# Kernel optimization log

Measured on AMD Instinct MI355X. Metric: run time of the kernel, lower is better.

Reference implementation:

```python
import jax, jax.numpy as jnp
import numpy as np

# Model constants (match init_kwargs)
B, V, NUM_NODES, NUM_RELS = 32, 20, 4000, 400
EMB, HID, L, N, E, OUT = 128, 128, 3, 32000, 256000, 128
DECAY = 0.03
EPS = 0.0  # self_attn eps, not trained


def setup_inputs() -> dict:
    key = jax.random.key(0)
    ks = jax.random.split(key, 20)
    s = 0.02
    return {
        "node_ids": jax.random.randint(ks[0], (N,), 0, NUM_NODES),
        "rel_ids": jax.random.randint(ks[1], (E,), 0, NUM_RELS),
        "edge_index": jax.random.randint(ks[2], (2, E), 0, N),
        "batch": jnp.sort(jax.random.randint(ks[3], (N,), 0, B)),
        "visit_node": jax.random.uniform(ks[4], (B, V, NUM_NODES), dtype=jnp.float32),
        "ehr_nodes": jax.random.uniform(ks[5], (B, NUM_NODES), dtype=jnp.float32),
        "node_emb": jax.random.normal(ks[6], (NUM_NODES, EMB), dtype=jnp.float32) * s,
        "rel_emb": jax.random.normal(ks[7], (NUM_RELS, EMB), dtype=jnp.float32) * s,
        "lin_w": jax.random.normal(ks[8], (HID, EMB), dtype=jnp.float32) * s,
        "lin_b": jnp.zeros((HID,), jnp.float32),
        "alpha_w": jax.random.normal(ks[9], (L, NUM_NODES, NUM_NODES), dtype=jnp.float32) * 0.002,
        "alpha_b": jnp.zeros((L, NUM_NODES), jnp.float32),
        "beta_w": jax.random.normal(ks[10], (L, 1, NUM_NODES), dtype=jnp.float32) * s,
        "beta_b": jnp.zeros((L, 1), jnp.float32),
        "wr_w": jax.random.normal(ks[11], (L, 1, HID), dtype=jnp.float32) * s,
        "wr_b": jnp.zeros((L, 1), jnp.float32),
        "nn_w": jax.random.normal(ks[12], (L, HID, HID), dtype=jnp.float32) * s,
        "nn_b": jnp.zeros((L, HID), jnp.float32),
        "mlp_w": jax.random.normal(ks[13], (OUT, 2 * HID), dtype=jnp.float32) * s,
        "mlp_b": jnp.zeros((OUT,), jnp.float32),
    }


def reference(node_ids, rel_ids, edge_index, batch, visit_node, ehr_nodes,
              node_emb, rel_emb, lin_w, lin_b, alpha_w, alpha_b, beta_w, beta_b,
              wr_w, wr_b, nn_w, nn_b, mlp_w, mlp_b):
    # visit decay weights lambda_j: (1, V, 1)
    lambda_j = jnp.exp(DECAY * (V - jnp.arange(V, dtype=jnp.float32))).reshape(1, V, 1)

    x = node_emb[node_ids] @ lin_w.T + lin_b          # (N, HID)
    edge_attr = rel_emb[rel_ids] @ lin_w.T + lin_b    # (E, HID)
    src, dst = edge_index[0], edge_index[1]
    nid_src = node_ids[src]
    b_src = batch[src]

    for l in range(L):
        # alpha: softmax over visit dim, (B, V, NUM_NODES)
        alpha = jax.nn.softmax(
            jnp.einsum('bvn,mn->bvm', visit_node, alpha_w[l]) + alpha_b[l], axis=1)
        # beta: (B, V, 1) with visit decay
        beta = jnp.tanh(
            jnp.einsum('bvn,on->bvo', visit_node, beta_w[l]) + beta_b[l]) * lambda_j
        attn = jnp.sum(alpha * beta, axis=1)          # (B, NUM_NODES)
        e_attn = attn[b_src, nid_src][:, None]        # (E, 1) per-edge attention

        # BiAttentionGNNConv message: relu(x_j * attn + W_R(edge_attr) * edge_attr)
        w_rel = edge_attr @ wr_w[l].T + wr_b[l]       # (E, 1)
        msg = jax.nn.relu(x[src] * e_attn + w_rel * edge_attr)
        agg = jax.ops.segment_sum(msg, dst, num_segments=N)  # scatter-add aggregate
        out = agg + (1.0 + EPS) * x                   # eps residual
        x = jax.nn.relu(out @ nn_w[l].T + nn_b[l])    # conv.nn Linear + outer relu

    # graph-level patient embedding: global mean pool over batch
    counts = jnp.maximum(
        jax.ops.segment_sum(jnp.ones((N, 1), x.dtype), batch, num_segments=B), 1.0)
    x_graph = jax.ops.segment_sum(x, batch, num_segments=B) / counts  # (B, HID)

    # node-level patient embedding: ehr multihot average of node embeddings
    x_node = (ehr_nodes @ node_emb) / jnp.sum(ehr_nodes, axis=1, keepdims=True)
    x_node = x_node @ lin_w.T + lin_b                 # (B, HID)

    logits = jnp.concatenate([x_graph, x_node], axis=1) @ mlp_w.T + mlp_b
    return logits
```

## Files before the change

### kernel.cpp

```cpp
#include <hip/hip_runtime.h>

namespace {

constexpr int kNodes = 4000;
constexpr int kRels  = 400;
constexpr int kB     = 32;
constexpr int kV     = 20;
constexpr int kN     = 32000;
constexpr int kE     = 256000;
constexpr int kH     = 128;
constexpr int kL     = 3;
constexpr int kMPad  = 4096;
constexpr int kKW    = 4000;
constexpr int kBV    = kB * kV;
constexpr int kNB    = 32;
constexpr int kChunk = kE / kNB;
constexpr int kHalf  = 16000;
constexpr int kPSeg  = 16;
constexpr int kESeg  = 32;

typedef __attribute__((ext_vector_type(8))) short bf16x8;
typedef __attribute__((ext_vector_type(4))) float f32x4;

__device__ inline unsigned short f2bf(float f){
  unsigned int u = __float_as_uint(f);
  u += 0x7FFFu + ((u >> 16) & 1u);
  return (unsigned short)(u >> 16);
}
__device__ inline float bf2f(unsigned short u){
  return __uint_as_float(((unsigned int)u) << 16);
}

__device__ inline void gload_lds16(const unsigned short* g, unsigned short* l){
  __builtin_amdgcn_global_load_lds(
      (const __attribute__((address_space(1))) unsigned int*)(g),
      (__attribute__((address_space(3))) unsigned int*)(l),
      16, 0, 0);
}


__global__ void transpose_kernel(const float* __restrict__ lin_w, const float* __restrict__ nn_w,
                                 float* __restrict__ lin_wT, float* __restrict__ nn_wT){
  int m = blockIdx.x;
  const float* in = (m == 0) ? lin_w : nn_w + (size_t)(m-1)*kH*kH;
  float* out      = (m == 0) ? lin_wT : nn_wT + (size_t)(m-1)*kH*kH;
  for (int i = threadIdx.x; i < kH*kH; i += blockDim.x){
    int r = i >> 7, c = i & (kH-1);
    out[c*kH + r] = in[i];
  }
}

__global__ __launch_bounds__(128) void proj_kernel(const float* __restrict__ node_emb,
    const float* __restrict__ rel_emb, const float* __restrict__ lin_wT,
    const float* __restrict__ lin_b, float* __restrict__ emb_lin, float* __restrict__ rel_lin){
  int row = blockIdx.x;
  const float* src; float* dst;
  if (row < kNodes){ src = node_emb + (size_t)row*kH; dst = emb_lin + (size_t)row*kH; }
  else             { src = rel_emb + (size_t)(row-kNodes)*kH; dst = rel_lin + (size_t)(row-kNodes)*kH; }
  __shared__ float rs[kH];
  int h = threadIdx.x;
  rs[h] = src[h];
  __syncthreads();
  float acc = lin_b[h];
#pragma unroll 8
  for (int k = 0; k < kH; k++) acc = fmaf(rs[k], lin_wT[k*kH + h], acc);
  dst[h] = acc;
}

__global__ void gather_x0_kernel(const int* __restrict__ node_ids,
                                 const float* __restrict__ emb_lin, float* __restrict__ x,
                                 unsigned short* __restrict__ xbf){
  int idx = blockIdx.x*256 + threadIdx.x;
  if (idx < kN*kH){
    int i = idx >> 7, c = idx & (kH-1);
    float v = emb_lin[(size_t)node_ids[i]*kH + c];
    x[idx] = v;
    xbf[idx] = f2bf(v);
  }
}

__global__ __launch_bounds__(128) void relterm_kernel(const float* __restrict__ rel_lin,
    const float* __restrict__ wr_w, const float* __restrict__ wr_b,
    unsigned short* __restrict__ relterm){
  int l = blockIdx.x / kRels, r = blockIdx.x % kRels;
  int t = threadIdx.x;
  float rl = rel_lin[(size_t)r*kH + t];
  __shared__ float red[kH];
  red[t] = rl * wr_w[l*kH + t];
  __syncthreads();
  for (int o = 64; o > 0; o >>= 1){
    if (t < o) red[t] += red[t+o];
    __syncthreads();
  }
  float w = red[0] + wr_b[l];
  relterm[((size_t)l*kRels + r)*kH + t] = f2bf(w * rl);
}


__global__ __launch_bounds__(256) void csr_hist_kernel(const int* __restrict__ dst,
    unsigned short* __restrict__ rank, unsigned int* __restrict__ hpart){
  __shared__ unsigned int hb[kHalf];
  int p = blockIdx.x;
  int base = blockIdx.y * kHalf;
  int t = threadIdx.x;
  for (int i = t; i < kHalf; i += 256) hb[i] = 0u;
  __syncthreads();
  for (int i = t; i < kChunk; i += 256){
    int e = p*kChunk + i;
    int d = dst[e];
    int rel = d - base;
    if ((unsigned)rel < (unsigned)kHalf){
      rank[e] = (unsigned short)atomicAdd(&hb[rel], 1u);
    }
  }
  __syncthreads();
  for (int i = t; i < kHalf; i += 256)
    hpart[(size_t)p*kN + base + i] = hb[i];
}

__global__ __launch_bounds__(256) void csr_col_kernel(unsigned int* __restrict__ hpart,
    int* __restrict__ deg){
  int bin = blockIdx.x*256 + threadIdx.x;
  if (bin >= kN) return;
  unsigned int s = 0;
#pragma unroll
  for (int p = 0; p < kNB; p++){
    size_t idx = (size_t)p*kN + bin;
    unsigned int v = hpart[idx];
    hpart[idx] = s;
    s += v;
  }
  deg[bin] = (int)s;
}

__global__ __launch_bounds__(256) void scanA_kernel(const int* __restrict__ deg,
    int* __restrict__ starts, int* __restrict__ bsum){
  __shared__ int buf[256];
  int gid = blockIdx.x*256 + threadIdx.x;
  int t = threadIdx.x;
  int v = (gid < kN) ? deg[gid] : 0;
  buf[t] = v;
  __syncthreads();
  for (int o = 1; o < 256; o <<= 1){
    int add = (t >= o) ? buf[t-o] : 0;
    __syncthreads();
    buf[t] += add;
    __syncthreads();
  }
  if (gid < kN) starts[gid] = buf[t] - v;
  if (t == 255) bsum[blockIdx.x] = buf[255];
}

__global__ __launch_bounds__(256) void scanC_kernel(int* __restrict__ starts,
    const int* __restrict__ bsum, int nblk){
  __shared__ int buf[128];
  int t = threadIdx.x;
  if (t < 128){
    int v = (t < nblk) ? bsum[t] : 0;
    buf[t] = v;
  }
  __syncthreads();
  for (int o = 1; o < 128; o <<= 1){
    int add = 0;
    if (t < 128 && t >= o) add = buf[t-o];
    __syncthreads();
    if (t < 128) buf[t] += add;
    __syncthreads();
  }
  int boff = (blockIdx.x > 0) ? buf[blockIdx.x - 1] : 0;
  int gid = blockIdx.x*256 + t;
  if (gid < kN) starts[gid] += boff;
  if (gid == kN-1) starts[kN] = kE;
}

__global__ __launch_bounds__(256) void csr_place_kernel(const int* __restrict__ dst,
    const int* __restrict__ src, const int* __restrict__ rel_ids,
    const int* __restrict__ starts, const unsigned int* __restrict__ colOff,
    const unsigned short* __restrict__ rank, int* __restrict__ epack){
  int blk = blockIdx.x;
  int p = blk >> 2;
  for (int i = threadIdx.x; i < 2000; i += 256){
    int e = blk*2000 + i;
    int d = dst[e];
    int pos = starts[d] + (int)colOff[(size_t)p*kN + d] + (int)rank[e];
    epack[pos] = src[e] | (rel_ids[e] << 15);
  }
}

__global__ void ub_kernel(const int* __restrict__ batch, int* __restrict__ ub){
  int j = threadIdx.x;
  if (j > kB) return;
  int lo = 0, hi = kN;
  while (lo < hi){
    int mid = (lo + hi) >> 1;
    if (batch[mid] < j) lo = mid + 1; else hi = mid;
  }
  ub[j] = lo;
}


__global__ __launch_bounds__(256) void visit_prep_kernel(const float* __restrict__ visit,
    const float* __restrict__ beta_w, const float* __restrict__ beta_b,
    unsigned short* __restrict__ visitbf, float* __restrict__ beta){
  int bv = blockIdx.x;
  int t = threadIdx.x;
  const float* row = visit + (size_t)bv*kKW;
  unsigned short* outr = visitbf + (size_t)bv*kKW;
  float d0 = 0.f, d1 = 0.f, d2 = 0.f;
  for (int i = t; i < kKW/4; i += 256){
    float4 v = *reinterpret_cast<const float4*>(row + i*4);
    unsigned int lo = ((unsigned int)f2bf(v.y) << 16) | f2bf(v.x);
    unsigned int hi = ((unsigned int)f2bf(v.w) << 16) | f2bf(v.z);
    *reinterpret_cast<uint2*>(outr + i*4) = uint2{lo, hi};
    float4 w0 = *reinterpret_cast<const float4*>(beta_w + i*4);
    float4 w1 = *reinterpret_cast<const float4*>(beta_w + kKW + i*4);
    float4 w2 = *reinterpret_cast<const float4*>(beta_w + 2*kKW + i*4);
    d0 = fmaf(v.x,w0.x, fmaf(v.y,w0.y, fmaf(v.z,w0.z, fmaf(v.w,w0.w, d0))));
    d1 = fmaf(v.x,w1.x, fmaf(v.y,w1.y, fmaf(v.z,w1.z, fmaf(v.w,w1.w, d1))));
    d2 = fmaf(v.x,w2.x, fmaf(v.y,w2.y, fmaf(v.z,w2.z, fmaf(v.w,w2.w, d2))));
  }
#pragma unroll
  for (int o = 32; o > 0; o >>= 1){
    d0 += __shfl_down(d0, o);
    d1 += __shfl_down(d1, o);
    d2 += __shfl_down(d2, o);
  }
  __shared__ float part[3][4];
  int wv = t >> 6, ln = t & 63;
  if (ln == 0){ part[0][wv] = d0; part[1][wv] = d1; part[2][wv] = d2; }
  __syncthreads();
  if (t < 3){
    float s = part[t][0] + part[t][1] + part[t][2] + part[t][3];
    int v = bv % kV;
    float lam = __expf(0.03f * (float)(kV - v));
    beta[t*kBV + bv] = tanhf(s + beta_b[t]) * lam;
  }
}

__global__ void cvtW_kernel(const float* __restrict__ W, unsigned short* __restrict__ out){
  int i = blockIdx.x*256 + threadIdx.x;
  constexpr int perL = kMPad*(kKW/8);
  if (i >= kL*perL) return;
  int l = i / perL;
  int rem = i - l*perL;
  int row = rem / (kKW/8);
  int col = (rem - row*(kKW/8)) * 8;
  unsigned short r[8];
  if (row < kNodes){
    const float* p = W + (size_t)l*kNodes*kNodes + (size_t)row*kKW + col;
    const float4 a = *reinterpret_cast<const float4*>(p);
    const float4 b = *reinterpret_cast<const float4*>(p + 4);
    r[0]=f2bf(a.x); r[1]=f2bf(a.y); r[2]=f2bf(a.z); r[3]=f2bf(a.w);
    r[4]=f2bf(b.x); r[5]=f2bf(b.y); r[6]=f2bf(b.z); r[7]=f2bf(b.w);
  } else {
    for (int q = 0; q < 8; q++) r[q] = 0;
  }
  *reinterpret_cast<uint4*>(out + (size_t)l*kMPad*kKW + (size_t)row*kKW + col)
      = *reinterpret_cast<uint4*>(r);
}

__global__ __launch_bounds__(256) void gemm_bt_bf16(const unsigned short* __restrict__ A,
    const unsigned short* __restrict__ Ball, unsigned short* __restrict__ Sbase){
  __shared__ unsigned short As[2][128*32];
  __shared__ unsigned short Bs[2][128*32];
  int wg = (blockIdx.x & 7)*120 + (blockIdx.x >> 3);
  int lz = wg / 160;
  int rem = wg - lz*160;
  int bn = rem / 5;
  int bm = rem - bn*5;
  int l = lz >> 1, z = lz & 1;
  const unsigned short* B = Ball + (size_t)l*kMPad*kKW;
  unsigned short* C = Sbase + (size_t)lz*kBV*kMPad;
  int tile0 = z ? 63 : 0;
  int nt    = z ? 62 : 63;

  int t = threadIdx.x;
  int lane = t & 63, wave = t >> 6;
  int wm = (wave >> 1) * 64, wn = (wave & 1) * 64;
  int r = lane & 15, g = lane >> 4;

  int ri = lane >> 2, s = lane & 3;
  int koff = ((s ^ ((ri >> 1) & 3)) << 3);
  const unsigned short* Ag = A + (size_t)(bm*128 + wave*32 + ri)*kKW + tile0*32 + koff;
  const unsigned short* Bg = B + (size_t)(bn*128 + wave*32 + ri)*kKW + tile0*32 + koff;
  const size_t rstep = (size_t)16*kKW;

  f32x4 acc[4][4];
#pragma unroll
  for (int i = 0; i < 4; i++)
#pragma unroll
    for (int j = 0; j < 4; j++) acc[i][j] = f32x4{0.f,0.f,0.f,0.f};

  auto STAGE = [&](int buf, int ts){
    const unsigned short* a = Ag + ts*32;
    const unsigned short* b = Bg + ts*32;
    gload_lds16(a,         &As[buf][(wave*32     )*32]);
    gload_lds16(a + rstep, &As[buf][(wave*32 + 16)*32]);
    gload_lds16(b,         &Bs[buf][(wave*32     )*32]);
    gload_lds16(b + rstep, &Bs[buf][(wave*32 + 16)*32]);
  };

  STAGE(0, 0);
  for (int ts = 0; ts < nt; ts++){
    int cur = ts & 1;
    __syncthreads();
    if (ts + 1 < nt) STAGE(cur ^ 1, ts + 1);
    bf16x8 af[4], bf[4];
#pragma unroll
    for (int i = 0; i < 4; i++){
      int arow = wm + i*16 + r;
      int brow = wn + i*16 + r;
      af[i] = *reinterpret_cast<const bf16x8*>(
          &As[cur][arow*32 + ((g ^ ((arow >> 1) & 3)) << 3)]);
      bf[i] = *reinterpret_cast<const bf16x8*>(
          &Bs[cur][brow*32 + ((g ^ ((brow >> 1) & 3)) << 3)]);
    }
#pragma unroll
    for (int i = 0; i < 4; i++)
#pragma unroll
      for (int j = 0; j < 4; j++)
        acc[i][j] = __builtin_amdgcn_mfma_f32_16x16x32_bf16(af[i], bf[j], acc[i][j], 0, 0, 0);
  }
#pragma unroll
  for (int i = 0; i < 4; i++)
#pragma unroll
    for (int j = 0; j < 4; j++){
      int row = bm*128 + wm + i*16 + g*4;
      int col = bn*128 + wn + j*16 + r;
#pragma unroll
      for (int q = 0; q < 4; q++)
        C[(size_t)(row + q)*kMPad + col] = f2bf(acc[i][j][q]);
    }
}

__global__ __launch_bounds__(256) void attn_kernel(const unsigned short* __restrict__ S,
    const float* __restrict__ beta, float* __restrict__ attn){
  int idx = blockIdx.x*256 + threadIdx.x;
  if (idx >= kL*kB*kNodes) return;
  int l = idx / (kB*kNodes);
  int rem = idx - l*(kB*kNodes);
  int b = rem / kNodes;
  int m = rem - b*kNodes;
  const unsigned short* S0 = S + (size_t)(l*2)*kBV*kMPad + (size_t)b*kV*kMPad + m;
  const unsigned short* S1 = S0 + (size_t)kBV*kMPad;
  float vals[kV];
  float mx = -1e30f;
#pragma unroll
  for (int v = 0; v < kV; v++){
    float s = bf2f(S0[(size_t)v*kMPad]) + bf2f(S1[(size_t)v*kMPad]);
    vals[v] = s; mx = fmaxf(mx, s);
  }
  float se = 0.f, ws = 0.f;
  const float* bp = beta + l*kBV + b*kV;
#pragma unroll
  for (int v = 0; v < kV; v++){ float e = __expf(vals[v] - mx); se += e; ws = fmaf(e, bp[v], ws); }
  attn[idx] = ws / se;
}

__global__ void edat_kernel(const int* __restrict__ epack, const int* __restrict__ batch,
    const int* __restrict__ node_ids, const float* __restrict__ attn,
    uint2* __restrict__ edat){
  int idx = blockIdx.x*256 + threadIdx.x;
  if (idx >= kL*kE) return;
  int l = idx / kE, p = idx - l*kE;
  int pk = epack[p];
  int s = pk & 0x7FFF;
  float at = attn[(size_t)l*kB*kNodes + (size_t)batch[s]*kNodes + node_ids[s]];
  edat[idx] = uint2{__float_as_uint(at), (unsigned int)pk};
}


__global__ __launch_bounds__(512) void aggnn_kernel(const int* __restrict__ starts,
    const uint2* __restrict__ edat_l, const unsigned short* __restrict__ relterm_l,
    const unsigned short* __restrict__ xbf_in, unsigned short* __restrict__ xbf_out,
    float* __restrict__ x, const float* __restrict__ nn_wT_l, const float* __restrict__ nn_b_l){
  __shared__ float rows[8][kH];
  int t = threadIdx.x;
  int wv = t >> 6, lane = t & 63;
  int node = blockIdx.x*8 + wv;
  int p0 = starts[node], p1 = starts[node+1];
  int c = lane*2;
  float a0 = 0.f, a1 = 0.f;

  float at_c = 0.f;
  unsigned int xv_c = 0u, rw_c = 0u;
  if (p0 < p1){
    uint2 ed = edat_l[p0];
    at_c = __uint_as_float(ed.x);
    int s0 = (int)(ed.y & 0x7FFFu);
    int r0 = (int)(ed.y >> 15);
    xv_c = *reinterpret_cast<const unsigned int*>(&xbf_in[(size_t)s0*kH + c]);
    rw_c = *reinterpret_cast<const unsigned int*>(&relterm_l[(size_t)r0*kH + c]);
  }
  for (int p = p0; p < p1; p++){
    float at_n = 0.f;
    unsigned int xv_n = 0u, rw_n = 0u;
    if (p + 1 < p1){
      uint2 ed = edat_l[p+1];
      at_n = __uint_as_float(ed.x);
      int sn = (int)(ed.y & 0x7FFFu);
      int rn = (int)(ed.y >> 15);
      xv_n = *reinterpret_cast<const unsigned int*>(&xbf_in[(size_t)sn*kH + c]);
      rw_n = *reinterpret_cast<const unsigned int*>(&relterm_l[(size_t)rn*kH + c]);
    }
    float x0 = __uint_as_float(xv_c << 16);
    float x1 = __uint_as_float(xv_c & 0xFFFF0000u);
    float r0 = __uint_as_float(rw_c << 16);
    float r1 = __uint_as_float(rw_c & 0xFFFF0000u);
    float m0 = fmaf(x0, at_c, r0); m0 = m0 > 0.f ? m0 : 0.f;
    float m1 = fmaf(x1, at_c, r1); m1 = m1 > 0.f ? m1 : 0.f;
    a0 += m0; a1 += m1;
    at_c = at_n; xv_c = xv_n; rw_c = rw_n;
  }
  size_t gi = (size_t)node*kH + c;
  rows[wv][c]   = a0 + x[gi];
  rows[wv][c+1] = a1 + x[gi+1];
  __syncthreads();
  int cc = t & 127;
  int r0 = (t >> 7) * 2;
  float acc0 = 0.f, acc1 = 0.f;
#pragma unroll 8
  for (int k = 0; k < kH; k++){
    float w = nn_wT_l[k*kH + cc];
    acc0 = fmaf(rows[r0  ][k], w, acc0);
    acc1 = fmaf(rows[r0+1][k], w, acc1);
  }
  float b = nn_b_l[cc];
  float o0 = fmaxf(acc0 + b, 0.f);
  float o1 = fmaxf(acc1 + b, 0.f);
  size_t n0 = (size_t)(blockIdx.x*8 + r0)*kH + cc;
  x[n0]        = o0;  xbf_out[n0]        = f2bf(o0);
  x[n0 + kH]   = o1;  xbf_out[n0 + kH]   = f2bf(o1);
}

__global__ __launch_bounds__(128) void readprep_kernel(const float* __restrict__ x,
    const int* __restrict__ ub, const float* __restrict__ ehr,
    const float* __restrict__ node_emb, float* __restrict__ pp,
    float* __restrict__ pn, float* __restrict__ ps){
  int s = blockIdx.x, b = blockIdx.y, c = threadIdx.x;
  if (s < kPSeg){
    int lo = ub[b], len = ub[b+1] - lo;
    int i0 = lo + (int)(((long long)len * s) / kPSeg);
    int i1 = lo + (int)(((long long)len * (s+1)) / kPSeg);
    float acc = 0.f;
    for (int i = i0; i < i1; i++) acc += x[(size_t)i*kH + c];
    pp[(size_t)(b*kPSeg + s)*kH + c] = acc;
  } else {
    int q = s - kPSeg;
    constexpr int seg = kNodes/kESeg;
    int n0 = q * seg;
    const float* ep = ehr + (size_t)b*kNodes + n0;
    const float* ne = node_emb + (size_t)n0*kH + c;
    float acc0 = 0.f, acc1 = 0.f, es = 0.f;
#pragma unroll 4
    for (int n = 0; n < seg - 1; n += 2){
      float e0 = ep[n], e1 = ep[n+1];
      es += e0 + e1;
      acc0 = fmaf(e0, ne[(size_t)n*kH], acc0);
      acc1 = fmaf(e1, ne[(size_t)(n+1)*kH], acc1);
    }
    {
      float e0 = ep[seg - 1];
      es += e0;
      acc0 = fmaf(e0, ne[(size_t)(seg - 1)*kH], acc0);
    }
    pn[(size_t)(b*kESeg + q)*kH + c] = acc0 + acc1;
    if (c == 0) ps[b*kESeg + q] = es;
  }
}

__global__ __launch_bounds__(128) void readout_kernel(const float* __restrict__ pp,
    const int* __restrict__ ub, const float* __restrict__ pn, const float* __restrict__ ps,
    const float* __restrict__ lin_wT, const float* __restrict__ lin_b,
    const float* __restrict__ mlp_w, const float* __restrict__ mlp_b,
    float* __restrict__ out){
  int b = blockIdx.x, h = threadIdx.x;
  __shared__ float v[2*kH];
  __shared__ float ts[kH];
  float s = 0.f;
#pragma unroll
  for (int q = 0; q < kPSeg; q++) s += pp[(size_t)(b*kPSeg + q)*kH + h];
  int len = ub[b+1] - ub[b]; if (len < 1) len = 1;
  v[h] = s / (float)len;
  float acc = 0.f, es = 0.f;
#pragma unroll
  for (int q = 0; q < kESeg; q++){
    acc += pn[(size_t)(b*kESeg + q)*kH + h];
    es  += ps[b*kESeg + q];
  }
  ts[h] = acc / es;
  __syncthreads();
  float r = lin_b[h];
#pragma unroll 8
  for (int k = 0; k < kH; k++) r = fmaf(ts[k], lin_wT[k*kH + h], r);
  v[kH + h] = r;
  __syncthreads();
  float o = mlp_b[h];
#pragma unroll 8
  for (int k = 0; k < 2*kH; k++) o = fmaf(v[k], mlp_w[(size_t)h*2*kH + k], o);
  out[b*kH + h] = o;
}

}

extern "C" void kernel_launch(void* const* d_in, const int* in_sizes, int n_in,
                              void* d_out, int out_size, void* d_ws, size_t ws_size,
                              hipStream_t stream){
  const int*   node_ids = (const int*)d_in[0];
  const int*   rel_ids  = (const int*)d_in[1];
  const int*   e_src    = (const int*)d_in[2];
  const int*   e_dst    = e_src + kE;
  const int*   batch    = (const int*)d_in[3];
  const float* visit    = (const float*)d_in[4];
  const float* ehr      = (const float*)d_in[5];
  const float* node_emb = (const float*)d_in[6];
  const float* rel_emb  = (const float*)d_in[7];
  const float* lin_w    = (const float*)d_in[8];
  const float* lin_b    = (const float*)d_in[9];
  const float* alpha_w  = (const float*)d_in[10];
  const float* beta_w   = (const float*)d_in[12];
  const float* beta_b   = (const float*)d_in[13];
  const float* wr_w     = (const float*)d_in[14];
  const float* wr_b     = (const float*)d_in[15];
  const float* nn_w     = (const float*)d_in[16];
  const float* nn_b     = (const float*)d_in[17];
  const float* mlp_w    = (const float*)d_in[18];
  const float* mlp_b    = (const float*)d_in[19];
  float* out = (float*)d_out;

  char* w = (char*)d_ws;
  auto alloc = [&](size_t bytes)->char*{
    char* p = w; w += (bytes + 255) & ~(size_t)255; return p;
  };
  int*   starts = (int*)  alloc((size_t)(kN+1)*4);
  int*   deg    = (int*)  alloc((size_t)kN*4);
  int*   bsum   = (int*)  alloc(256*4);
  int*   ub     = (int*)  alloc((kB+1)*4);
  int*   epack  = (int*)  alloc((size_t)kE*4);
  unsigned short* rank = (unsigned short*)alloc((size_t)kE*2);
  unsigned int* hpart  = (unsigned int*)alloc((size_t)kNB*kN*4);
  float* embLin = (float*)alloc((size_t)kNodes*kH*4);
  float* relLin = (float*)alloc((size_t)kRels*kH*4);
  unsigned short* relterm = (unsigned short*)alloc((size_t)kL*kRels*kH*2);
  float* linwT  = (float*)alloc((size_t)kH*kH*4);
  float* nnwT   = (float*)alloc((size_t)kL*kH*kH*4);
  float* x      = (float*)alloc((size_t)kN*kH*4);
  unsigned short* xbfA = (unsigned short*)alloc((size_t)kN*kH*2);
  unsigned short* xbfB = (unsigned short*)alloc((size_t)kN*kH*2);
  unsigned short* visitbf = (unsigned short*)alloc((size_t)kBV*kKW*2);
  unsigned short* awbf    = (unsigned short*)alloc((size_t)kL*kMPad*kKW*2);
  unsigned short* S       = (unsigned short*)alloc((size_t)kL*2*kBV*kMPad*2);
  float* attn   = (float*)alloc((size_t)kL*kB*kNodes*4);
  uint2* edat   = (uint2*)alloc((size_t)kL*kE*8);
  float* beta   = (float*)alloc((size_t)kL*kBV*4);
  float* pp     = (float*)alloc((size_t)kB*kPSeg*kH*4);
  float* pn     = (float*)alloc((size_t)kB*kESeg*kH*4);
  float* ps     = (float*)alloc((size_t)kB*kESeg*4);
  if ((size_t)(w - (char*)d_ws) > ws_size) return;

  transpose_kernel<<<4, 256, 0, stream>>>(lin_w, nn_w, linwT, nnwT);
  proj_kernel<<<kNodes + kRels, 128, 0, stream>>>(node_emb, rel_emb, linwT, lin_b, embLin, relLin);
  gather_x0_kernel<<<(kN*kH)/256, 256, 0, stream>>>(node_ids, embLin, x, xbfA);
  relterm_kernel<<<kL*kRels, 128, 0, stream>>>(relLin, wr_w, wr_b, relterm);

  csr_hist_kernel<<<dim3(kNB, 2), 256, 0, stream>>>(e_dst, rank, hpart);
  csr_col_kernel<<<(kN+255)/256, 256, 0, stream>>>(hpart, deg);
  scanA_kernel<<<(kN+255)/256, 256, 0, stream>>>(deg, starts, bsum);
  scanC_kernel<<<(kN+255)/256, 256, 0, stream>>>(starts, bsum, (kN+255)/256);
  csr_place_kernel<<<128, 256, 0, stream>>>(e_dst, e_src, rel_ids, starts, hpart, rank, epack);
  ub_kernel<<<1, 64, 0, stream>>>(batch, ub);

  visit_prep_kernel<<<kBV, 256, 0, stream>>>(visit, beta_w, beta_b, visitbf, beta);
  cvtW_kernel<<<(kL*kMPad*(kKW/8) + 255)/256, 256, 0, stream>>>(alpha_w, awbf);
  gemm_bt_bf16<<<960, 256, 0, stream>>>(visitbf, awbf, S);
  attn_kernel<<<(kL*kB*kNodes + 255)/256, 256, 0, stream>>>(S, beta, attn);
  edat_kernel<<<(kL*kE + 255)/256, 256, 0, stream>>>(epack, batch, node_ids, attn, edat);

  unsigned short* xin = xbfA;
  unsigned short* xout = xbfB;
  for (int l = 0; l < kL; l++){
    aggnn_kernel<<<kN/8, 512, 0, stream>>>(starts,
        edat + (size_t)l*kE, relterm + (size_t)l*kRels*kH,
        xin, xout, x, nnwT + (size_t)l*kH*kH, nn_b + (size_t)l*kH);
    unsigned short* tmp = xin; xin = xout; xout = tmp;
  }

  readprep_kernel<<<dim3(kPSeg + kESeg, kB), 128, 0, stream>>>(x, ub, ehr, node_emb, pp, pn, ps);
  readout_kernel<<<kB, 128, 0, stream>>>(pp, ub, pn, ps, linwT, lin_b, mlp_w, mlp_b, out);
}
```

Measured before the change: 507.9 us.

## Fuse alpha_w bf16 conversion into GEMM by loading fp32 tiles directly

Removes the separate cvtW pass that converted the 3x4000x4000 fp32 alpha weights into a padded bf16 buffer. The GEMM now stages fp32 B tiles into LDS with a new swizzle and converts them to bf16 in registers with v_cvt_pk_bf16_f32 before the MFMA. This saves one full read plus a bf16 write and re-read of the large weight tensor. In exchange the GEMM reads fp32 (twice the bytes per B tile), uses double the B LDS footprint, and clamps out-of-range rows to row 0 instead of zero padding.

```diff
diff --git a/kernel.cpp b/kernel.cpp
--- a/kernel.cpp
+++ b/kernel.cpp
@@ -30,8 +30,19 @@
 __device__ inline float bf2f(unsigned short u){
   return __uint_as_float(((unsigned int)u) << 16);
 }
+__device__ inline unsigned int cvt_pk_bf16(float lo, float hi){
+  unsigned int r;
+  asm("v_cvt_pk_bf16_f32 %0, %1, %2" : "=v"(r) : "v"(lo), "v"(hi));
+  return r;
+}
 
 __device__ inline void gload_lds16(const unsigned short* g, unsigned short* l){
+  __builtin_amdgcn_global_load_lds(
+      (const __attribute__((address_space(1))) unsigned int*)(g),
+      (__attribute__((address_space(3))) unsigned int*)(l),
+      16, 0, 0);
+}
+__device__ inline void gload_lds16f(const float* g, float* l){
   __builtin_amdgcn_global_load_lds(
       (const __attribute__((address_space(1))) unsigned int*)(g),
       (__attribute__((address_space(3))) unsigned int*)(l),
@@ -237,39 +248,17 @@
   }
 }
 
-__global__ void cvtW_kernel(const float* __restrict__ W, unsigned short* __restrict__ out){
-  int i = blockIdx.x*256 + threadIdx.x;
-  constexpr int perL = kMPad*(kKW/8);
-  if (i >= kL*perL) return;
-  int l = i / perL;
-  int rem = i - l*perL;
-  int row = rem / (kKW/8);
-  int col = (rem - row*(kKW/8)) * 8;
-  unsigned short r[8];
-  if (row < kNodes){
-    const float* p = W + (size_t)l*kNodes*kNodes + (size_t)row*kKW + col;
-    const float4 a = *reinterpret_cast<const float4*>(p);
-    const float4 b = *reinterpret_cast<const float4*>(p + 4);
-    r[0]=f2bf(a.x); r[1]=f2bf(a.y); r[2]=f2bf(a.z); r[3]=f2bf(a.w);
-    r[4]=f2bf(b.x); r[5]=f2bf(b.y); r[6]=f2bf(b.z); r[7]=f2bf(b.w);
-  } else {
-    for (int q = 0; q < 8; q++) r[q] = 0;
-  }
-  *reinterpret_cast<uint4*>(out + (size_t)l*kMPad*kKW + (size_t)row*kKW + col)
-      = *reinterpret_cast<uint4*>(r);
-}
-
 __global__ __launch_bounds__(256) void gemm_bt_bf16(const unsigned short* __restrict__ A,
-    const unsigned short* __restrict__ Ball, unsigned short* __restrict__ Sbase){
+    const float* __restrict__ alpha, unsigned short* __restrict__ Sbase){
   __shared__ unsigned short As[2][128*32];
-  __shared__ unsigned short Bs[2][128*32];
+  __shared__ float Bs[2][128*32];
   int wg = (blockIdx.x & 7)*120 + (blockIdx.x >> 3);
   int lz = wg / 160;
   int rem = wg - lz*160;
   int bn = rem / 5;
   int bm = rem - bn*5;
   int l = lz >> 1, z = lz & 1;
-  const unsigned short* B = Ball + (size_t)l*kMPad*kKW;
+  const float* B = alpha + (size_t)l*kNodes*kNodes;
   unsigned short* C = Sbase + (size_t)lz*kBV*kMPad;
   int tile0 = z ? 63 : 0;
   int nt    = z ? 62 : 63;
@@ -279,11 +268,18 @@
   int wm = (wave >> 1) * 64, wn = (wave & 1) * 64;
   int r = lane & 15, g = lane >> 4;
 
-  int ri = lane >> 2, s = lane & 3;
-  int koff = ((s ^ ((ri >> 1) & 3)) << 3);
-  const unsigned short* Ag = A + (size_t)(bm*128 + wave*32 + ri)*kKW + tile0*32 + koff;
-  const unsigned short* Bg = B + (size_t)(bn*128 + wave*32 + ri)*kKW + tile0*32 + koff;
-  const size_t rstep = (size_t)16*kKW;
+  int ri4 = lane >> 2, s4 = lane & 3;
+  int koffA = ((s4 ^ ((ri4 >> 1) & 3)) << 3);
+  const unsigned short* Ag = A + (size_t)(bm*128 + wave*32 + ri4)*kKW + tile0*32 + koffA;
+  const size_t rstepA = (size_t)16*kKW;
+
+  int ri8 = lane >> 3, s8 = lane & 7;
+  int koffB = ((s8 ^ ri8) << 2);
+  int brow0 = bn*128 + wave*32 + ri8;
+  const float* Bg0 = B + (size_t)(brow0      < kNodes ? brow0      : 0)*kKW + tile0*32 + koffB;
+  const float* Bg1 = B + (size_t)(brow0 + 8  < kNodes ? brow0 + 8  : 0)*kKW + tile0*32 + koffB;
+  const float* Bg2 = B + (size_t)(brow0 + 16 < kNodes ? brow0 + 16 : 0)*kKW + tile0*32 + koffB;
+  const float* Bg3 = B + (size_t)(brow0 + 24 < kNodes ? brow0 + 24 : 0)*kKW + tile0*32 + koffB;
 
   f32x4 acc[4][4];
 #pragma unroll
@@ -293,11 +289,12 @@
 
   auto STAGE = [&](int buf, int ts){
     const unsigned short* a = Ag + ts*32;
-    const unsigned short* b = Bg + ts*32;
-    gload_lds16(a,         &As[buf][(wave*32     )*32]);
-    gload_lds16(a + rstep, &As[buf][(wave*32 + 16)*32]);
-    gload_lds16(b,         &Bs[buf][(wave*32     )*32]);
-    gload_lds16(b + rstep, &Bs[buf][(wave*32 + 16)*32]);
+    gload_lds16(a,          &As[buf][(wave*32     )*32]);
+    gload_lds16(a + rstepA, &As[buf][(wave*32 + 16)*32]);
+    gload_lds16f(Bg0 + ts*32, &Bs[buf][(wave*32     )*32]);
+    gload_lds16f(Bg1 + ts*32, &Bs[buf][(wave*32 +  8)*32]);
+    gload_lds16f(Bg2 + ts*32, &Bs[buf][(wave*32 + 16)*32]);
+    gload_lds16f(Bg3 + ts*32, &Bs[buf][(wave*32 + 24)*32]);
   };
 
   STAGE(0, 0);
@@ -309,11 +306,19 @@
 #pragma unroll
     for (int i = 0; i < 4; i++){
       int arow = wm + i*16 + r;
-      int brow = wn + i*16 + r;
       af[i] = *reinterpret_cast<const bf16x8*>(
           &As[cur][arow*32 + ((g ^ ((arow >> 1) & 3)) << 3)]);
-      bf[i] = *reinterpret_cast<const bf16x8*>(
-          &Bs[cur][brow*32 + ((g ^ ((brow >> 1) & 3)) << 3)]);
+      int brow = wn + i*16 + r;
+      int key = brow & 7;
+      const float* bp = &Bs[cur][brow*32];
+      float4 lo = *reinterpret_cast<const float4*>(bp + ((((g<<1)    ) ^ key) << 2));
+      float4 hi = *reinterpret_cast<const float4*>(bp + ((((g<<1) | 1) ^ key) << 2));
+      union { unsigned int u[4]; bf16x8 v; } bb;
+      bb.u[0] = cvt_pk_bf16(lo.x, lo.y);
+      bb.u[1] = cvt_pk_bf16(lo.z, lo.w);
+      bb.u[2] = cvt_pk_bf16(hi.x, hi.y);
+      bb.u[3] = cvt_pk_bf16(hi.z, hi.w);
+      bf[i] = bb.v;
     }
 #pragma unroll
     for (int i = 0; i < 4; i++)
@@ -548,7 +553,6 @@
   unsigned short* xbfA = (unsigned short*)alloc((size_t)kN*kH*2);
   unsigned short* xbfB = (unsigned short*)alloc((size_t)kN*kH*2);
   unsigned short* visitbf = (unsigned short*)alloc((size_t)kBV*kKW*2);
-  unsigned short* awbf    = (unsigned short*)alloc((size_t)kL*kMPad*kKW*2);
   unsigned short* S       = (unsigned short*)alloc((size_t)kL*2*kBV*kMPad*2);
   float* attn   = (float*)alloc((size_t)kL*kB*kNodes*4);
   uint2* edat   = (uint2*)alloc((size_t)kL*kE*8);
@@ -571,8 +575,7 @@
   ub_kernel<<<1, 64, 0, stream>>>(batch, ub);
 
   visit_prep_kernel<<<kBV, 256, 0, stream>>>(visit, beta_w, beta_b, visitbf, beta);
-  cvtW_kernel<<<(kL*kMPad*(kKW/8) + 255)/256, 256, 0, stream>>>(alpha_w, awbf);
-  gemm_bt_bf16<<<960, 256, 0, stream>>>(visitbf, awbf, S);
+  gemm_bt_bf16<<<960, 256, 0, stream>>>(visitbf, alpha_w, S);
   attn_kernel<<<(kL*kB*kNodes + 255)/256, 256, 0, stream>>>(S, beta, attn);
   edat_kernel<<<(kL*kE + 255)/256, 256, 0, stream>>>(epack, batch, node_ids, attn, edat);
 
```

New measurement: 561.7 us. 10.6% more time.
